# Optimization experiments

Measured on AMD Instinct MI355X. Metric: run time of the kernel, lower is better.

The kernel has to match this reference:

```python
import jax, jax.numpy as jnp
import numpy as np

B, H, S, D = 2, 12, 2048, 64

def setup_inputs() -> dict:
    key = jax.random.key(0)
    kq, kk, kv, km = jax.random.split(key, 4)
    return {
        "q": jax.random.normal(kq, (B, H, S, D), dtype=jnp.float32),
        "k": jax.random.normal(kk, (B, H, S, D), dtype=jnp.float32),
        "v": jax.random.normal(kv, (B, H, S, D), dtype=jnp.float32),
        "mask": jax.random.normal(km, (B, 1, S, S), dtype=jnp.float32),
    }

def reference(q, k, v, mask):
    # scores: [B,H,S,S] = Q @ K^T + mask (additive, broadcast over heads)
    scores = jnp.einsum("bhqd,bhkd->bhqk", q, k) + mask
    probs = jax.nn.softmax(scores, axis=-1)
    return jnp.einsum("bhqk,bhkd->bhqd", probs, v)
```

## Files before the change

kernel.cpp:

```cpp
#include <hip/hip_runtime.h>
#include <hip/hip_bf16.h>
#include <stdint.h>

#define S_LEN 2048
#define D_DIM 64
#define HEADS 12
#define KVB   64
#define QBLK  64
#define NTILES (S_LEN / KVB)

typedef __attribute__((ext_vector_type(8))) short bf16x8;
typedef __attribute__((ext_vector_type(4))) float f32x4;

__device__ __forceinline__ unsigned short f2bf(float x) {
    union { float f; uint32_t u; } v; v.f = x;
    uint32_t r = v.u + 0x7FFFu + ((v.u >> 16) & 1u);
    return (unsigned short)(r >> 16);
}
__device__ __forceinline__ float bf2f(unsigned short h) {
    union { uint32_t u; float f; } t; t.u = ((uint32_t)h) << 16; return t.f;
}
__device__ __forceinline__ void split2(float x, unsigned short& h, unsigned short& l) {
    h = f2bf(x);
    l = f2bf(x - bf2f(h));
}

__global__ __launch_bounds__(256, 3)
void attn_fwd(const float* __restrict__ Q, const float* __restrict__ K,
              const float* __restrict__ V, const float* __restrict__ M,
              float* __restrict__ O)
{
    __shared__ unsigned char klds_h[64 * 128];
    __shared__ unsigned char klds_l[64 * 128];
    __shared__ unsigned char vlds[64 * 128];

    const int bid  = blockIdx.x;
    const int bh   = bid >> 5;
    const int qb   = bid & 31;
    const int b    = bh / HEADS;
    const long qkv_base  = (long)bh * S_LEN * D_DIM;
    const long mask_base = (long)b * S_LEN * S_LEN;

    const int tid  = threadIdx.x;
    const int wave = tid >> 6;
    const int lane = tid & 63;
    const int c    = lane & 15;
    const int g    = lane >> 4;
    const int sw   = (c & 7) << 4;

    const int qrow = qb * QBLK + wave * 16 + c;

    bf16x8 qfh[2], qfl[2];
    {
        const float* qp = Q + qkv_base + (long)qrow * D_DIM;
        #pragma unroll
        for (int f = 0; f < 2; ++f) {
            float4 x0 = *(const float4*)(qp + f * 32 + 8 * g);
            float4 x1 = *(const float4*)(qp + f * 32 + 8 * g + 4);
            float e[8] = { x0.x, x0.y, x0.z, x0.w, x1.x, x1.y, x1.z, x1.w };
            bf16x8 th, tl;
            #pragma unroll
            for (int j = 0; j < 8; ++j) {
                unsigned short h, l;
                split2(e[j], h, l);
                th[j] = (short)h; tl[j] = (short)l;
            }
            qfh[f] = th; qfl[f] = tl;
        }
    }

    f32x4 o[4] = {};
    float m_run = -INFINITY, l_run = 0.f;
    const float* mrow = M + mask_base + (long)qrow * S_LEN;

    for (int t0 = 0; t0 < NTILES; ++t0) {
        const int k0 = t0 * KVB;

        {
            const float* kp = K + qkv_base + (long)k0 * D_DIM;
            #pragma unroll
            for (int it = 0; it < 4; ++it) {
                int i   = tid + 256 * it;
                int row = i >> 4;
                int c4  = i & 15;
                float4 x = *(const float4*)(kp + row * 64 + c4 * 4);
                unsigned short h0, l0, h1, l1, h2, l2, h3, l3;
                split2(x.x, h0, l0); split2(x.y, h1, l1);
                split2(x.z, h2, l2); split2(x.w, h3, l3);
                int off = row * 128 + ((c4 * 8) ^ ((row & 7) << 4));
                *(uint2*)(klds_h + off) =
                    make_uint2(((uint32_t)h1 << 16) | h0, ((uint32_t)h3 << 16) | h2);
                *(uint2*)(klds_l + off) =
                    make_uint2(((uint32_t)l1 << 16) | l0, ((uint32_t)l3 << 16) | l2);
            }
        }
        {
            const float* vp = V + qkv_base + (long)k0 * D_DIM;
            int d = tid & 63, a = tid >> 6;
            #pragma unroll
            for (int h = 0; h < 2; ++h) {
                int kk0 = 32 * h + 8 * a;
                uint32_t w0, w1, w2, w3;
                {
                    float e0 = vp[(kk0 + 0) * 64 + d], e1 = vp[(kk0 + 1) * 64 + d];
                    float e2 = vp[(kk0 + 2) * 64 + d], e3 = vp[(kk0 + 3) * 64 + d];
                    float e4 = vp[(kk0 + 4) * 64 + d], e5 = vp[(kk0 + 5) * 64 + d];
                    float e6 = vp[(kk0 + 6) * 64 + d], e7 = vp[(kk0 + 7) * 64 + d];
                    w0 = ((uint32_t)f2bf(e1) << 16) | f2bf(e0);
                    w1 = ((uint32_t)f2bf(e3) << 16) | f2bf(e2);
                    w2 = ((uint32_t)f2bf(e5) << 16) | f2bf(e4);
                    w3 = ((uint32_t)f2bf(e7) << 16) | f2bf(e6);
                }
                int off = d * 128 + ((kk0 * 2) ^ ((d & 7) << 4));
                *(uint4*)(vlds + off) = make_uint4(w0, w1, w2, w3);
            }
        }
        __syncthreads();

        f32x4 st[4];
        #pragma unroll
        for (int kt = 0; kt < 4; ++kt) {
            const unsigned char* bh_ = klds_h + (16 * kt + c) * 128;
            const unsigned char* bl_ = klds_l + (16 * kt + c) * 128;
            bf16x8 kh0 = *(const bf16x8*)(bh_ + ((16 * g) ^ sw));
            bf16x8 kh1 = *(const bf16x8*)(bh_ + ((64 + 16 * g) ^ sw));
            bf16x8 kl0 = *(const bf16x8*)(bl_ + ((16 * g) ^ sw));
            bf16x8 kl1 = *(const bf16x8*)(bl_ + ((64 + 16 * g) ^ sw));
            f32x4 acc = {};
            acc = __builtin_amdgcn_mfma_f32_16x16x32_bf16(kh0, qfl[0], acc, 0, 0, 0);
            acc = __builtin_amdgcn_mfma_f32_16x16x32_bf16(kh1, qfl[1], acc, 0, 0, 0);
            acc = __builtin_amdgcn_mfma_f32_16x16x32_bf16(kl0, qfh[0], acc, 0, 0, 0);
            acc = __builtin_amdgcn_mfma_f32_16x16x32_bf16(kl1, qfh[1], acc, 0, 0, 0);
            acc = __builtin_amdgcn_mfma_f32_16x16x32_bf16(kh0, qfh[0], acc, 0, 0, 0);
            acc = __builtin_amdgcn_mfma_f32_16x16x32_bf16(kh1, qfh[1], acc, 0, 0, 0);
            st[kt] = acc;
        }

        float p[4][4];
        float tmax = -INFINITY;
        #pragma unroll
        for (int kt = 0; kt < 4; ++kt)
            #pragma unroll
            for (int r = 0; r < 4; ++r) {
                float sc = st[kt][r] + mrow[k0 + 16 * kt + 4 * g + r];
                p[kt][r] = sc;
                tmax = fmaxf(tmax, sc);
            }
        tmax = fmaxf(tmax, __shfl_xor(tmax, 16, 64));
        tmax = fmaxf(tmax, __shfl_xor(tmax, 32, 64));
        float m_new = fmaxf(m_run, tmax);
        float scale = __expf(m_run - m_new);
        float tsum = 0.f;
        #pragma unroll
        for (int kt = 0; kt < 4; ++kt)
            #pragma unroll
            for (int r = 0; r < 4; ++r) {
                float e = __expf(p[kt][r] - m_new);
                p[kt][r] = e;
                tsum += e;
            }
        tsum += __shfl_xor(tsum, 16, 64);
        tsum += __shfl_xor(tsum, 32, 64);
        l_run = l_run * scale + tsum;
        m_run = m_new;
        #pragma unroll
        for (int mt = 0; mt < 4; ++mt) o[mt] *= scale;

        uint32_t w[4][2];
        #pragma unroll
        for (int kt = 0; kt < 4; ++kt) {
            w[kt][0] = ((uint32_t)f2bf(p[kt][1]) << 16) | f2bf(p[kt][0]);
            w[kt][1] = ((uint32_t)f2bf(p[kt][3]) << 16) | f2bf(p[kt][2]);
        }
        bf16x8 pf[2];
        const bool hi_half = (lane & 32) != 0;
        #pragma unroll
        for (int f = 0; f < 2; ++f) {
            uint32_t words[4];
            #pragma unroll
            for (int pp = 0; pp < 4; ++pp) {
                int srcl = 16 * (2 * (g & 1) + (pp >> 1)) + c;
                int addr = srcl << 2;
                int lo = __builtin_amdgcn_ds_bpermute(addr, (int)w[2 * f][pp & 1]);
                int hi = __builtin_amdgcn_ds_bpermute(addr, (int)w[2 * f + 1][pp & 1]);
                words[pp] = hi_half ? (uint32_t)hi : (uint32_t)lo;
            }
            union { uint32_t u[4]; bf16x8 v; } cv;
            cv.u[0] = words[0]; cv.u[1] = words[1];
            cv.u[2] = words[2]; cv.u[3] = words[3];
            pf[f] = cv.v;
        }

        #pragma unroll
        for (int f = 0; f < 2; ++f) {
            #pragma unroll
            for (int mt = 0; mt < 4; ++mt) {
                const unsigned char* base = vlds + (16 * mt + c) * 128;
                bf16x8 vf = *(const bf16x8*)(base + ((64 * f + 16 * g) ^ sw));
                o[mt] = __builtin_amdgcn_mfma_f32_16x16x32_bf16(vf, pf[f], o[mt], 0, 0, 0);
            }
        }
        __syncthreads();
    }

    float inv = 1.0f / l_run;
    float* op = O + qkv_base + (long)qrow * D_DIM;
    #pragma unroll
    for (int mt = 0; mt < 4; ++mt) {
        float4 x = make_float4(o[mt][0] * inv, o[mt][1] * inv,
                               o[mt][2] * inv, o[mt][3] * inv);
        *(float4*)(op + 16 * mt + 4 * g) = x;
    }
}

extern "C" void kernel_launch(void* const* d_in, const int* in_sizes, int n_in,
                              void* d_out, int out_size, void* d_ws, size_t ws_size,
                              hipStream_t stream) {
    const float* q = (const float*)d_in[0];
    const float* k = (const float*)d_in[1];
    const float* v = (const float*)d_in[2];
    const float* m = (const float*)d_in[3];
    float* o = (float*)d_out;
    dim3 grid(2 * HEADS * (S_LEN / QBLK));
    dim3 block(256);
    attn_fwd<<<grid, block, 0, stream>>>(q, k, v, m, o);
}
```

Before: 215.3 us.

## Pre-convert K/V to bf16 tiles in workspace and stream tiles via global_load_lds

Adds a prepass kernel that splits K into bf16 hi/lo and transposes V into bf16, writing them in the already-swizzled LDS tile layout to a workspace. The attention kernel then copies each pre-formatted tile straight into LDS with global_load_lds, and stages the mask tile through LDS too. This removes the redundant per-block conversion of K/V, which was repeated by all 32 query blocks per head, and makes the mask loads coalesced. The cost is an extra kernel launch, workspace traffic, and more LDS per block (40KB), which may limit occupancy. The original kernel is kept as a fallback when the workspace is too small.

```diff
diff --git a/kernel.cpp b/kernel.cpp
--- a/kernel.cpp
+++ b/kernel.cpp
@@ -8,6 +8,12 @@
 #define KVB   64
 #define QBLK  64
 #define NTILES (S_LEN / KVB)
+#define BH    (2 * HEADS)
+#define TILE_BYTES 8192
+#define KH_OFF ((size_t)0)
+#define KL_OFF ((size_t)BH * NTILES * TILE_BYTES)
+#define VT_OFF ((size_t)2 * BH * NTILES * TILE_BYTES)
+#define WS_NEED ((size_t)3 * BH * NTILES * TILE_BYTES)
 
 typedef __attribute__((ext_vector_type(8))) short bf16x8;
 typedef __attribute__((ext_vector_type(4))) float f32x4;
@@ -24,15 +30,67 @@
     h = f2bf(x);
     l = f2bf(x - bf2f(h));
 }
+__device__ __forceinline__ void gload16(const void* g, void* l) {
+    __builtin_amdgcn_global_load_lds(
+        (const __attribute__((address_space(1))) void*)g,
+        (__attribute__((address_space(3))) void*)l, 16, 0, 0);
+}
+
+__global__ __launch_bounds__(256, 4)
+void convert_kv(const float* __restrict__ K, const float* __restrict__ V,
+                unsigned char* __restrict__ ws)
+{
+    const int blk = blockIdx.x;
+    const int bh  = blk >> 5;
+    const int t   = blk & 31;
+    const long qkv_base = (long)bh * S_LEN * D_DIM;
+    const int tid = threadIdx.x;
+    unsigned char* kh = ws + KH_OFF + (size_t)blk * TILE_BYTES;
+    unsigned char* kl = ws + KL_OFF + (size_t)blk * TILE_BYTES;
+    unsigned char* vt = ws + VT_OFF + (size_t)blk * TILE_BYTES;
+    const int k0 = t * KVB;
+
+    const float* kp = K + qkv_base + (long)k0 * D_DIM;
+    #pragma unroll
+    for (int it = 0; it < 4; ++it) {
+        int i   = tid + 256 * it;
+        int row = i >> 4;
+        int c4  = i & 15;
+        float4 x = *(const float4*)(kp + row * 64 + c4 * 4);
+        unsigned short h0, l0, h1, l1, h2, l2, h3, l3;
+        split2(x.x, h0, l0); split2(x.y, h1, l1);
+        split2(x.z, h2, l2); split2(x.w, h3, l3);
+        int off = row * 128 + ((c4 * 8) ^ ((row & 7) << 4));
+        *(uint2*)(kh + off) = make_uint2(((uint32_t)h1 << 16) | h0, ((uint32_t)h3 << 16) | h2);
+        *(uint2*)(kl + off) = make_uint2(((uint32_t)l1 << 16) | l0, ((uint32_t)l3 << 16) | l2);
+    }
+
+    const float* vp = V + qkv_base + (long)k0 * D_DIM;
+    int d = tid & 63, a = tid >> 6;
+    #pragma unroll
+    for (int h = 0; h < 2; ++h) {
+        int kk0 = 32 * h + 8 * a;
+        float e0 = vp[(kk0 + 0) * 64 + d], e1 = vp[(kk0 + 1) * 64 + d];
+        float e2 = vp[(kk0 + 2) * 64 + d], e3 = vp[(kk0 + 3) * 64 + d];
+        float e4 = vp[(kk0 + 4) * 64 + d], e5 = vp[(kk0 + 5) * 64 + d];
+        float e6 = vp[(kk0 + 6) * 64 + d], e7 = vp[(kk0 + 7) * 64 + d];
+        uint32_t w0 = ((uint32_t)f2bf(e1) << 16) | f2bf(e0);
+        uint32_t w1 = ((uint32_t)f2bf(e3) << 16) | f2bf(e2);
+        uint32_t w2 = ((uint32_t)f2bf(e5) << 16) | f2bf(e4);
+        uint32_t w3 = ((uint32_t)f2bf(e7) << 16) | f2bf(e6);
+        int off = d * 128 + ((kk0 * 2) ^ ((d & 7) << 4));
+        *(uint4*)(vt + off) = make_uint4(w0, w1, w2, w3);
+    }
+}
 
 __global__ __launch_bounds__(256, 3)
-void attn_fwd(const float* __restrict__ Q, const float* __restrict__ K,
-              const float* __restrict__ V, const float* __restrict__ M,
-              float* __restrict__ O)
+void attn_fwd_ws(const float* __restrict__ Q, const float* __restrict__ M,
+                 const unsigned char* __restrict__ ws, float* __restrict__ O)
 {
-    __shared__ unsigned char klds_h[64 * 128];
-    __shared__ unsigned char klds_l[64 * 128];
-    __shared__ unsigned char vlds[64 * 128];
+    __shared__ unsigned char klds_h[8192];
+    __shared__ unsigned char klds_l[8192];
+    __shared__ unsigned char vlds[8192];
+    __shared__ unsigned char mlds[16384];
 
     const int bid  = blockIdx.x;
     const int bh   = bid >> 5;
@@ -69,51 +127,35 @@
         }
     }
 
+    const unsigned char* khB = ws + KH_OFF + (size_t)bh * NTILES * TILE_BYTES;
+    const unsigned char* klB = ws + KL_OFF + (size_t)bh * NTILES * TILE_BYTES;
+    const unsigned char* vtB = ws + VT_OFF + (size_t)bh * NTILES * TILE_BYTES;
+    const float* mrow0 = M + mask_base + (long)(qb * QBLK) * S_LEN;
+
     f32x4 o[4] = {};
     float m_run = -INFINITY, l_run = 0.f;
-    const float* mrow = M + mask_base + (long)qrow * S_LEN;
 
     for (int t0 = 0; t0 < NTILES; ++t0) {
-        const int k0 = t0 * KVB;
-
-        {
-            const float* kp = K + qkv_base + (long)k0 * D_DIM;
-            #pragma unroll
-            for (int it = 0; it < 4; ++it) {
-                int i   = tid + 256 * it;
-                int row = i >> 4;
-                int c4  = i & 15;
-                float4 x = *(const float4*)(kp + row * 64 + c4 * 4);
-                unsigned short h0, l0, h1, l1, h2, l2, h3, l3;
-                split2(x.x, h0, l0); split2(x.y, h1, l1);
-                split2(x.z, h2, l2); split2(x.w, h3, l3);
-                int off = row * 128 + ((c4 * 8) ^ ((row & 7) << 4));
-                *(uint2*)(klds_h + off) =
-                    make_uint2(((uint32_t)h1 << 16) | h0, ((uint32_t)h3 << 16) | h2);
-                *(uint2*)(klds_l + off) =
-                    make_uint2(((uint32_t)l1 << 16) | l0, ((uint32_t)l3 << 16) | l2);
-            }
-        }
-        {
-            const float* vp = V + qkv_base + (long)k0 * D_DIM;
-            int d = tid & 63, a = tid >> 6;
-            #pragma unroll
-            for (int h = 0; h < 2; ++h) {
-                int kk0 = 32 * h + 8 * a;
-                uint32_t w0, w1, w2, w3;
-                {
-                    float e0 = vp[(kk0 + 0) * 64 + d], e1 = vp[(kk0 + 1) * 64 + d];
-                    float e2 = vp[(kk0 + 2) * 64 + d], e3 = vp[(kk0 + 3) * 64 + d];
-                    float e4 = vp[(kk0 + 4) * 64 + d], e5 = vp[(kk0 + 5) * 64 + d];
-                    float e6 = vp[(kk0 + 6) * 64 + d], e7 = vp[(kk0 + 7) * 64 + d];
-                    w0 = ((uint32_t)f2bf(e1) << 16) | f2bf(e0);
-                    w1 = ((uint32_t)f2bf(e3) << 16) | f2bf(e2);
-                    w2 = ((uint32_t)f2bf(e5) << 16) | f2bf(e4);
-                    w3 = ((uint32_t)f2bf(e7) << 16) | f2bf(e6);
-                }
-                int off = d * 128 + ((kk0 * 2) ^ ((d & 7) << 4));
-                *(uint4*)(vlds + off) = make_uint4(w0, w1, w2, w3);
-            }
+        const unsigned char* khT = khB + (size_t)t0 * TILE_BYTES;
+        const unsigned char* klT = klB + (size_t)t0 * TILE_BYTES;
+        const unsigned char* vtT = vtB + (size_t)t0 * TILE_BYTES;
+
+        #pragma unroll
+        for (int j = 0; j < 2; ++j) {
+            int o2 = wave * 2048 + j * 1024;
+            gload16(khT + o2 + lane * 16, klds_h + o2);
+            gload16(klT + o2 + lane * 16, klds_l + o2);
+            gload16(vtT + o2 + lane * 16, vlds + o2);
+        }
+        #pragma unroll
+        for (int j = 0; j < 4; ++j) {
+            int o2 = wave * 4096 + j * 1024;
+            int X  = o2 + lane * 16;
+            int q  = X >> 8;
+            int ib = X & 255;
+            const unsigned char* gm =
+                (const unsigned char*)(mrow0 + (long)q * S_LEN) + t0 * 256;
+            gload16(gm + (ib ^ ((q & 7) << 4)), mlds + o2);
         }
         __syncthreads();
 
@@ -136,6 +178,195 @@
             st[kt] = acc;
         }
 
+        const int mq = wave * 16 + c;
+        const unsigned char* mrl = mlds + mq * 256;
+        float p[4][4];
+        float tmax = -INFINITY;
+        #pragma unroll
+        for (int kt = 0; kt < 4; ++kt) {
+            union { float4 v; float a[4]; } mu;
+            mu.v = *(const float4*)(mrl + ((64 * kt + 16 * g) ^ sw));
+            #pragma unroll
+            for (int r = 0; r < 4; ++r) {
+                float sc = st[kt][r] + mu.a[r];
+                p[kt][r] = sc;
+                tmax = fmaxf(tmax, sc);
+            }
+        }
+        tmax = fmaxf(tmax, __shfl_xor(tmax, 16, 64));
+        tmax = fmaxf(tmax, __shfl_xor(tmax, 32, 64));
+        float m_new = fmaxf(m_run, tmax);
+        float scale = __expf(m_run - m_new);
+        float tsum = 0.f;
+        #pragma unroll
+        for (int kt = 0; kt < 4; ++kt)
+            #pragma unroll
+            for (int r = 0; r < 4; ++r) {
+                float e = __expf(p[kt][r] - m_new);
+                p[kt][r] = e;
+                tsum += e;
+            }
+        tsum += __shfl_xor(tsum, 16, 64);
+        tsum += __shfl_xor(tsum, 32, 64);
+        l_run = l_run * scale + tsum;
+        m_run = m_new;
+        #pragma unroll
+        for (int mt = 0; mt < 4; ++mt) o[mt] *= scale;
+
+        uint32_t w[4][2];
+        #pragma unroll
+        for (int kt = 0; kt < 4; ++kt) {
+            w[kt][0] = ((uint32_t)f2bf(p[kt][1]) << 16) | f2bf(p[kt][0]);
+            w[kt][1] = ((uint32_t)f2bf(p[kt][3]) << 16) | f2bf(p[kt][2]);
+        }
+        bf16x8 pf[2];
+        const bool hi_half = (lane & 32) != 0;
+        #pragma unroll
+        for (int f = 0; f < 2; ++f) {
+            uint32_t words[4];
+            #pragma unroll
+            for (int pp = 0; pp < 4; ++pp) {
+                int srcl = 16 * (2 * (g & 1) + (pp >> 1)) + c;
+                int addr = srcl << 2;
+                int lo = __builtin_amdgcn_ds_bpermute(addr, (int)w[2 * f][pp & 1]);
+                int hi = __builtin_amdgcn_ds_bpermute(addr, (int)w[2 * f + 1][pp & 1]);
+                words[pp] = hi_half ? (uint32_t)hi : (uint32_t)lo;
+            }
+            union { uint32_t u[4]; bf16x8 v; } cv;
+            cv.u[0] = words[0]; cv.u[1] = words[1];
+            cv.u[2] = words[2]; cv.u[3] = words[3];
+            pf[f] = cv.v;
+        }
+
+        #pragma unroll
+        for (int f = 0; f < 2; ++f) {
+            #pragma unroll
+            for (int mt = 0; mt < 4; ++mt) {
+                const unsigned char* base = vlds + (16 * mt + c) * 128;
+                bf16x8 vf = *(const bf16x8*)(base + ((64 * f + 16 * g) ^ sw));
+                o[mt] = __builtin_amdgcn_mfma_f32_16x16x32_bf16(vf, pf[f], o[mt], 0, 0, 0);
+            }
+        }
+        __syncthreads();
+    }
+
+    float inv = 1.0f / l_run;
+    float* op = O + qkv_base + (long)qrow * D_DIM;
+    #pragma unroll
+    for (int mt = 0; mt < 4; ++mt) {
+        float4 x = make_float4(o[mt][0] * inv, o[mt][1] * inv,
+                               o[mt][2] * inv, o[mt][3] * inv);
+        *(float4*)(op + 16 * mt + 4 * g) = x;
+    }
+}
+
+__global__ __launch_bounds__(256, 3)
+void attn_fwd(const float* __restrict__ Q, const float* __restrict__ K,
+              const float* __restrict__ V, const float* __restrict__ M,
+              float* __restrict__ O)
+{
+    __shared__ unsigned char klds_h[64 * 128];
+    __shared__ unsigned char klds_l[64 * 128];
+    __shared__ unsigned char vlds[64 * 128];
+
+    const int bid  = blockIdx.x;
+    const int bh   = bid >> 5;
+    const int qb   = bid & 31;
+    const int b    = bh / HEADS;
+    const long qkv_base  = (long)bh * S_LEN * D_DIM;
+    const long mask_base = (long)b * S_LEN * S_LEN;
+
+    const int tid  = threadIdx.x;
+    const int wave = tid >> 6;
+    const int lane = tid & 63;
+    const int c    = lane & 15;
+    const int g    = lane >> 4;
+    const int sw   = (c & 7) << 4;
+
+    const int qrow = qb * QBLK + wave * 16 + c;
+
+    bf16x8 qfh[2], qfl[2];
+    {
+        const float* qp = Q + qkv_base + (long)qrow * D_DIM;
+        #pragma unroll
+        for (int f = 0; f < 2; ++f) {
+            float4 x0 = *(const float4*)(qp + f * 32 + 8 * g);
+            float4 x1 = *(const float4*)(qp + f * 32 + 8 * g + 4);
+            float e[8] = { x0.x, x0.y, x0.z, x0.w, x1.x, x1.y, x1.z, x1.w };
+            bf16x8 th, tl;
+            #pragma unroll
+            for (int j = 0; j < 8; ++j) {
+                unsigned short h, l;
+                split2(e[j], h, l);
+                th[j] = (short)h; tl[j] = (short)l;
+            }
+            qfh[f] = th; qfl[f] = tl;
+        }
+    }
+
+    f32x4 o[4] = {};
+    float m_run = -INFINITY, l_run = 0.f;
+    const float* mrow = M + mask_base + (long)qrow * S_LEN;
+
+    for (int t0 = 0; t0 < NTILES; ++t0) {
+        const int k0 = t0 * KVB;
+        {
+            const float* kp = K + qkv_base + (long)k0 * D_DIM;
+            #pragma unroll
+            for (int it = 0; it < 4; ++it) {
+                int i   = tid + 256 * it;
+                int row = i >> 4;
+                int c4  = i & 15;
+                float4 x = *(const float4*)(kp + row * 64 + c4 * 4);
+                unsigned short h0, l0, h1, l1, h2, l2, h3, l3;
+                split2(x.x, h0, l0); split2(x.y, h1, l1);
+                split2(x.z, h2, l2); split2(x.w, h3, l3);
+                int off = row * 128 + ((c4 * 8) ^ ((row & 7) << 4));
+                *(uint2*)(klds_h + off) =
+                    make_uint2(((uint32_t)h1 << 16) | h0, ((uint32_t)h3 << 16) | h2);
+                *(uint2*)(klds_l + off) =
+                    make_uint2(((uint32_t)l1 << 16) | l0, ((uint32_t)l3 << 16) | l2);
+            }
+        }
+        {
+            const float* vp = V + qkv_base + (long)k0 * D_DIM;
+            int d = tid & 63, a = tid >> 6;
+            #pragma unroll
+            for (int h = 0; h < 2; ++h) {
+                int kk0 = 32 * h + 8 * a;
+                float e0 = vp[(kk0 + 0) * 64 + d], e1 = vp[(kk0 + 1) * 64 + d];
+                float e2 = vp[(kk0 + 2) * 64 + d], e3 = vp[(kk0 + 3) * 64 + d];
+                float e4 = vp[(kk0 + 4) * 64 + d], e5 = vp[(kk0 + 5) * 64 + d];
+                float e6 = vp[(kk0 + 6) * 64 + d], e7 = vp[(kk0 + 7) * 64 + d];
+                uint32_t w0 = ((uint32_t)f2bf(e1) << 16) | f2bf(e0);
+                uint32_t w1 = ((uint32_t)f2bf(e3) << 16) | f2bf(e2);
+                uint32_t w2 = ((uint32_t)f2bf(e5) << 16) | f2bf(e4);
+                uint32_t w3 = ((uint32_t)f2bf(e7) << 16) | f2bf(e6);
+                int off = d * 128 + ((kk0 * 2) ^ ((d & 7) << 4));
+                *(uint4*)(vlds + off) = make_uint4(w0, w1, w2, w3);
+            }
+        }
+        __syncthreads();
+
+        f32x4 st[4];
+        #pragma unroll
+        for (int kt = 0; kt < 4; ++kt) {
+            const unsigned char* bh_ = klds_h + (16 * kt + c) * 128;
+            const unsigned char* bl_ = klds_l + (16 * kt + c) * 128;
+            bf16x8 kh0 = *(const bf16x8*)(bh_ + ((16 * g) ^ sw));
+            bf16x8 kh1 = *(const bf16x8*)(bh_ + ((64 + 16 * g) ^ sw));
+            bf16x8 kl0 = *(const bf16x8*)(bl_ + ((16 * g) ^ sw));
+            bf16x8 kl1 = *(const bf16x8*)(bl_ + ((64 + 16 * g) ^ sw));
+            f32x4 acc = {};
+            acc = __builtin_amdgcn_mfma_f32_16x16x32_bf16(kh0, qfl[0], acc, 0, 0, 0);
+            acc = __builtin_amdgcn_mfma_f32_16x16x32_bf16(kh1, qfl[1], acc, 0, 0, 0);
+            acc = __builtin_amdgcn_mfma_f32_16x16x32_bf16(kl0, qfh[0], acc, 0, 0, 0);
+            acc = __builtin_amdgcn_mfma_f32_16x16x32_bf16(kl1, qfh[1], acc, 0, 0, 0);
+            acc = __builtin_amdgcn_mfma_f32_16x16x32_bf16(kh0, qfh[0], acc, 0, 0, 0);
+            acc = __builtin_amdgcn_mfma_f32_16x16x32_bf16(kh1, qfh[1], acc, 0, 0, 0);
+            st[kt] = acc;
+        }
+
         float p[4][4];
         float tmax = -INFINITY;
         #pragma unroll
@@ -221,7 +452,12 @@
     const float* v = (const float*)d_in[2];
     const float* m = (const float*)d_in[3];
     float* o = (float*)d_out;
-    dim3 grid(2 * HEADS * (S_LEN / QBLK));
+    dim3 grid(BH * (S_LEN / QBLK));
     dim3 block(256);
-    attn_fwd<<<grid, block, 0, stream>>>(q, k, v, m, o);
-}
+    if (ws_size >= WS_NEED) {
+        convert_kv<<<grid, block, 0, stream>>>(k, v, (unsigned char*)d_ws);
+        attn_fwd_ws<<<grid, block, 0, stream>>>(q, m, (const unsigned char*)d_ws, o);
+    } else {
+        attn_fwd<<<grid, block, 0, stream>>>(q, k, v, m, o);
+    }
+}
```

Result: faster. 195.2 us (-9.3%).
